# Kernel optimization log

Measured on AMD Instinct MI355X. Metric: run time of the kernel, lower is better.

The kernel has to match this reference:

```python
import jax, jax.numpy as jnp
import numpy as np

LN_EPS = 1e-5

def setup_inputs() -> dict:
    key = jax.random.key(0)
    ks = jax.random.split(key, 12)
    B, T, R, Ds = 4, 128, 64, 128
    N = 2048
    d_id = 128
    max_neurons, max_regions, max_eids = 2048, 128, 256
    U = jax.random.normal(ks[0], (B, T, R, Ds), dtype=jnp.float32)
    neuron_regions = jax.random.randint(ks[1], (B, N), 0, max_regions, dtype=jnp.int32)
    eids = jax.random.randint(ks[2], (B,), 0, max_eids, dtype=jnp.int32)
    r_map = jax.random.randint(ks[3], (max_regions,), 0, R, dtype=jnp.int32)
    s = 0.02
    neuron_slot = jax.random.normal(ks[4], (max_neurons, d_id), dtype=jnp.float32) * s
    region_emb = jax.random.normal(ks[5], (max_regions, d_id), dtype=jnp.float32) * s
    eid_emb = jax.random.normal(ks[6], (max_eids, d_id), dtype=jnp.float32) * s
    ln_gamma = jnp.ones((d_id,), dtype=jnp.float32)
    ln_beta = jnp.zeros((d_id,), dtype=jnp.float32)
    W1 = jax.random.normal(ks[7], (d_id, 2 * Ds), dtype=jnp.float32) * (1.0 / np.sqrt(d_id))
    b1 = jnp.zeros((2 * Ds,), dtype=jnp.float32)
    W2 = jax.random.normal(ks[8], (2 * Ds, Ds + 1), dtype=jnp.float32) * (1.0 / np.sqrt(2 * Ds))
    b2 = jnp.zeros((Ds + 1,), dtype=jnp.float32)  # nn.init.zeros_ on hyper[-1].bias
    return {"U": U, "neuron_regions": neuron_regions, "eids": eids, "r_map": r_map,
            "neuron_slot": neuron_slot, "region_emb": region_emb, "eid_emb": eid_emb,
            "ln_gamma": ln_gamma, "ln_beta": ln_beta, "W1": W1, "b1": b1, "W2": W2, "b2": b2}


def reference(U, neuron_regions, eids, r_map, neuron_slot, region_emb, eid_emb,
              ln_gamma, ln_beta, W1, b1, W2, b2):
    B, T, R, Ds = U.shape
    N = neuron_regions.shape[1]
    # neuron identity embedding: slot + region (+ eid)
    nr = jnp.clip(neuron_regions, 0, region_emb.shape[0] - 1)
    e = neuron_slot[:N][None, :, :] + region_emb[nr]                      # [B,N,d_id]
    e = e + eid_emb[jnp.clip(eids, 0, eid_emb.shape[0] - 1)][:, None, :]
    # hyper-MLP: LayerNorm -> Linear -> GELU(exact) -> Linear
    mu = e.mean(-1, keepdims=True)
    var = ((e - mu) ** 2).mean(-1, keepdims=True)
    h = (e - mu) * jax.lax.rsqrt(var + LN_EPS) * ln_gamma + ln_beta
    h = jax.nn.gelu(h @ W1 + b1, approximate=False)
    wb = h @ W2 + b2                                                      # [B,N,Ds+1]
    w = wb[..., :Ds]                                                      # [B,N,Ds]
    bias = wb[..., Ds]                                                    # [B,N]
    # region-indexed gather + weighted reduce
    local_r = r_map[jnp.clip(neuron_regions, 0, r_map.shape[0] - 1)]      # [B,N]
    lr_safe = jnp.clip(local_r, 0, None)
    idx = jnp.broadcast_to(lr_safe[:, None, :, None], (B, T, N, Ds))
    U_neur = jnp.take_along_axis(U, idx, axis=2)                          # [B,T,N,Ds]
    pred = jnp.einsum('btnd,bnd->btn', U_neur, w) + bias[:, None, :]
    pred = jnp.where((local_r < 0)[:, None, :], jnp.zeros_like(pred), pred)
    return pred
```

## Files before the change

### kernel.cpp

```cpp
#include <hip/hip_runtime.h>
#include <hip/hip_bf16.h>
#include <math.h>

#define DEV __device__ __forceinline__

typedef __attribute__((ext_vector_type(8))) short short8v;
typedef __attribute__((ext_vector_type(4))) float f32x4;

DEV unsigned short f2bf(float x) {
    unsigned u = __float_as_uint(x);
    return (unsigned short)((u + 0x7fffu + ((u >> 16) & 1u)) >> 16);
}
DEV unsigned pack2(float lo, float hi) {
    return ((unsigned)f2bf(hi) << 16) | (unsigned)f2bf(lo);
}
DEV f32x4 mfma16(short8v a, short8v b, f32x4 c) {
    return __builtin_amdgcn_mfma_f32_16x16x32_bf16(a, b, c, 0, 0, 0);
}

DEV float gelu_fast(float x) {
    const float z  = x * 0.70710678118654752f;
    const float az = fabsf(z);
    const float t  = __builtin_amdgcn_rcpf(fmaf(0.3275911f, az, 1.0f));
    float p = fmaf(t, 1.061405429f, -1.453152027f);
    p = fmaf(t, p, 1.421413741f);
    p = fmaf(t, p, -0.284496736f);
    p = fmaf(t, p, 0.254829592f);
    p = p * t;
    const float E = __builtin_amdgcn_exp2f(z * z * -1.4426950408889634f);
    const float erf_az = fmaf(-p, E, 1.0f);
    const float erf_z  = copysignf(erf_az, z);
    const float hx = 0.5f * x;
    return fmaf(hx, erf_z, hx);
}

#define NN 2048

__global__ __launch_bounds__(256, 1) void prep_kernel(
    const float* __restrict__ W1, const float* __restrict__ W2,
    const int* __restrict__ r_map, const int* __restrict__ neuron_regions,
    unsigned short* __restrict__ W1T, unsigned short* __restrict__ W2T,
    float* __restrict__ w2col, int* __restrict__ order, int* __restrict__ offs)
{
    __shared__ __align__(16) float T[32][33];
    __shared__ int hist[65], starts[66], cursor[65];
    const int tid = threadIdx.x;
    const int bid = blockIdx.x;

    if (bid < 32) {
        const int tr = bid >> 3, tc = bid & 7;
#pragma unroll
        for (int p = 0; p < 4; p++) {
            const int i = p * 8 + (tid >> 5), j = tid & 31;
            T[i][j] = W1[(tr * 32 + i) * 256 + tc * 32 + j];
        }
        __syncthreads();
#pragma unroll
        for (int p = 0; p < 4; p++) {
            const int i = p * 8 + (tid >> 5), j = tid & 31;
            W1T[(tc * 32 + i) * 128 + tr * 32 + j] = f2bf(T[j][i]);
        }
    } else if (bid < 64) {
        const int bb = bid - 32, tr = bb >> 2, tc = bb & 3;
#pragma unroll
        for (int p = 0; p < 4; p++) {
            const int i = p * 8 + (tid >> 5), j = tid & 31;
            T[i][j] = W2[(tr * 32 + i) * 129 + tc * 32 + j];
        }
        __syncthreads();
#pragma unroll
        for (int p = 0; p < 4; p++) {
            const int i = p * 8 + (tid >> 5), j = tid & 31;
            W2T[(tc * 32 + i) * 256 + tr * 32 + j] = f2bf(T[j][i]);
        }
    } else if (bid == 64) {
        w2col[tid] = W2[tid * 129 + 128];
    } else {
        const int b = bid - 65;
        for (int i = tid; i < 65; i += 256) hist[i] = 0;
        __syncthreads();
        for (int n = tid; n < NN; n += 256) {
            int nr = min(max(neuron_regions[b * NN + n], 0), 127);
            int lr = r_map[nr];
            int bin = (lr < 0) ? 64 : min(lr, 63);
            atomicAdd(&hist[bin], 1);
        }
        __syncthreads();
        if (tid == 0) {
            int run = 0;
            for (int i = 0; i < 65; i++) { starts[i] = run; cursor[i] = run; run += hist[i]; }
            starts[65] = run;
        }
        __syncthreads();
        for (int i = tid; i < 66; i += 256) offs[b * 66 + i] = starts[i];
        for (int n = tid; n < NN; n += 256) {
            int nr = min(max(neuron_regions[b * NN + n], 0), 127);
            int lr = r_map[nr];
            int bin = (lr < 0) ? 64 : min(lr, 63);
            int pos = atomicAdd(&cursor[bin], 1);
            order[b * NN + pos] = n;
        }
    }
}

__global__ __launch_bounds__(256, 2) void p1_kernel(
    const int* __restrict__ neuron_regions, const int* __restrict__ eids,
    const float* __restrict__ neuron_slot, const float* __restrict__ region_emb,
    const float* __restrict__ eid_emb, const float* __restrict__ ln_gamma,
    const float* __restrict__ ln_beta, const float* __restrict__ b1,
    const float* __restrict__ b2, const unsigned short* __restrict__ W1T,
    const unsigned short* __restrict__ W2T, const float* __restrict__ w2col,
    unsigned short* __restrict__ w_ws, float* __restrict__ bias_ws)
{
    __shared__ __align__(16) unsigned short hT[16][136];
    __shared__ __align__(16) unsigned short H1[16][264];
    __shared__ float biasp[16];
    const int tid = threadIdx.x;
    const int row0 = blockIdx.x * 16;
    if (tid < 16) biasp[tid] = 0.f;

    {
        const int rr = tid >> 4, q = tid & 15;
        const int row = row0 + rr;
        const int b = row >> 11, n = row & (NN - 1);
        int nr = min(max(neuron_regions[b * NN + n], 0), 127);
        int eid = min(max(eids[b], 0), 255);
        const float* ns = neuron_slot + n * 128 + q * 8;
        const float* re = region_emb + nr * 128 + q * 8;
        const float* ee = eid_emb + eid * 128 + q * 8;
        float e[8];
        {
            float4 a0 = *(const float4*)ns, a1 = *(const float4*)(ns + 4);
            float4 c0 = *(const float4*)re, c1 = *(const float4*)(re + 4);
            float4 d0 = *(const float4*)ee, d1 = *(const float4*)(ee + 4);
            e[0] = a0.x + c0.x + d0.x; e[1] = a0.y + c0.y + d0.y;
            e[2] = a0.z + c0.z + d0.z; e[3] = a0.w + c0.w + d0.w;
            e[4] = a1.x + c1.x + d1.x; e[5] = a1.y + c1.y + d1.y;
            e[6] = a1.z + c1.z + d1.z; e[7] = a1.w + c1.w + d1.w;
        }
        float s = 0.f, s2 = 0.f;
#pragma unroll
        for (int i = 0; i < 8; i++) { s += e[i]; s2 += e[i] * e[i]; }
        s += __shfl_xor(s, 1);  s2 += __shfl_xor(s2, 1);
        s += __shfl_xor(s, 2);  s2 += __shfl_xor(s2, 2);
        s += __shfl_xor(s, 4);  s2 += __shfl_xor(s2, 4);
        s += __shfl_xor(s, 8);  s2 += __shfl_xor(s2, 8);
        const float mu = s * (1.f / 128.f);
        const float var = s2 * (1.f / 128.f) - mu * mu;
        const float rstd = rsqrtf(var + 1e-5f);
        float4 g0 = *(const float4*)(ln_gamma + q * 8), g1 = *(const float4*)(ln_gamma + q * 8 + 4);
        float4 t0 = *(const float4*)(ln_beta + q * 8),  t1 = *(const float4*)(ln_beta + q * 8 + 4);
        float gm[8] = {g0.x, g0.y, g0.z, g0.w, g1.x, g1.y, g1.z, g1.w};
        float bt[8] = {t0.x, t0.y, t0.z, t0.w, t1.x, t1.y, t1.z, t1.w};
        float h[8];
#pragma unroll
        for (int i = 0; i < 8; i++) h[i] = (e[i] - mu) * rstd * gm[i] + bt[i];
        uint4 pk;
        pk.x = pack2(h[0], h[1]); pk.y = pack2(h[2], h[3]);
        pk.z = pack2(h[4], h[5]); pk.w = pack2(h[6], h[7]);
        *(uint4*)&hT[rr][q * 8] = pk;
    }
    __syncthreads();

    const int wv = tid >> 6, l = tid & 63;
    const int lr = l & 15, lh = l >> 4;

    short8v afr[4];
#pragma unroll
    for (int ks = 0; ks < 4; ks++)
        afr[ks] = *(const short8v*)&hT[lr][ks * 32 + lh * 8];

    float pb[4] = {0.f, 0.f, 0.f, 0.f};
#pragma unroll
    for (int nt = 0; nt < 4; nt++) {
        const int n = wv * 64 + nt * 16 + lr;
        short8v bfr[4];
#pragma unroll
        for (int ks = 0; ks < 4; ks++)
            bfr[ks] = *(const short8v*)(W1T + n * 128 + ks * 32 + lh * 8);
        const float bb = b1[n];
        const float w2cv = w2col[n];
        f32x4 a; a.x = bb; a.y = bb; a.z = bb; a.w = bb;
#pragma unroll
        for (int ks = 0; ks < 4; ks++) a = mfma16(afr[ks], bfr[ks], a);
#pragma unroll
        for (int j = 0; j < 4; j++) {
            const float g = gelu_fast(a[j]);
            H1[lh * 4 + j][n] = f2bf(g);
            pb[j] += g * w2cv;
        }
    }
#pragma unroll
    for (int j = 0; j < 4; j++) {
        pb[j] += __shfl_xor(pb[j], 1);
        pb[j] += __shfl_xor(pb[j], 2);
        pb[j] += __shfl_xor(pb[j], 4);
        pb[j] += __shfl_xor(pb[j], 8);
    }
    if (lr == 0) {
#pragma unroll
        for (int j = 0; j < 4; j++) atomicAdd(&biasp[lh * 4 + j], pb[j]);
    }
    __syncthreads();

    if (tid < 16) bias_ws[row0 + tid] = biasp[tid] + b2[128];

    short8v a2[8];
#pragma unroll
    for (int ks = 0; ks < 8; ks++)
        a2[ks] = *(const short8v*)&H1[lr][ks * 32 + lh * 8];

    f32x4 acc2[2];
#pragma unroll
    for (int nt = 0; nt < 2; nt++) {
        const int n = wv * 32 + nt * 16 + lr;
        short8v bf[8];
#pragma unroll
        for (int ks = 0; ks < 8; ks++)
            bf[ks] = *(const short8v*)(W2T + n * 256 + ks * 32 + lh * 8);
        const float bb = b2[n];
        f32x4 a; a.x = bb; a.y = bb; a.z = bb; a.w = bb;
#pragma unroll
        for (int ks = 0; ks < 8; ks++) a = mfma16(a2[ks], bf[ks], a);
        acc2[nt] = a;
    }

    __syncthreads();
#pragma unroll
    for (int nt = 0; nt < 2; nt++) {
        const int n = wv * 32 + nt * 16 + lr;
#pragma unroll
        for (int j = 0; j < 4; j++)
            hT[lh * 4 + j][n] = f2bf(acc2[nt][j]);
    }
    __syncthreads();
    {
        const int r = tid >> 4, c = tid & 15;
        uint4 v = *(const uint4*)&hT[r][c * 8];
        *(uint4*)(w_ws + (row0 + r) * 128 + c * 8) = v;
    }
}

__global__ __launch_bounds__(256, 1) void p2_kernel(
    const float* __restrict__ U, const int* __restrict__ order,
    const int* __restrict__ offs, const unsigned short* __restrict__ w_ws,
    const float* __restrict__ bias_ws, float* __restrict__ out)
{
    __shared__ __align__(16) unsigned short Ubf[32][136];
    __shared__ __align__(16) unsigned short Bt[32][136];
    __shared__ int nidS[32];
    __shared__ float biasS[32];
    const int tid = threadIdx.x;
    const int bid = blockIdx.x;

    if (bid >= 1024) {
        const int b = bid - 1024;
        const int s64 = offs[b * 66 + 64], s65 = offs[b * 66 + 65];
        const int cnt = s65 - s64;
        for (int idx = tid; idx < cnt * 128; idx += 256) {
            const int j = idx >> 7, t = idx & 127;
            const int n = order[b * NN + s64 + j];
            out[(size_t)(b * 128 + t) * NN + n] = 0.f;
        }
        return;
    }

    const int b = bid >> 8, rem = bid & 255;
    const int slot = rem >> 2, tq = rem & 3;
    const int t0 = tq * 32;
    const int s0 = offs[b * 66 + slot], s1 = offs[b * 66 + slot + 1];
    const int cnt = s1 - s0;
    if (cnt <= 0) return;

    {
        const int t = tid >> 3, q = tid & 7;
        const float* src = U + ((size_t)((b * 128 + t0 + t) * 64 + slot)) * 128 + q * 16;
        unsigned short* dst = &Ubf[t][q * 16];
        float4 v0 = ((const float4*)src)[0], v1 = ((const float4*)src)[1];
        float4 v2 = ((const float4*)src)[2], v3 = ((const float4*)src)[3];
        uint4 pkA, pkB;
        pkA.x = pack2(v0.x, v0.y); pkA.y = pack2(v0.z, v0.w);
        pkA.z = pack2(v1.x, v1.y); pkA.w = pack2(v1.z, v1.w);
        pkB.x = pack2(v2.x, v2.y); pkB.y = pack2(v2.z, v2.w);
        pkB.z = pack2(v3.x, v3.y); pkB.w = pack2(v3.z, v3.w);
        ((uint4*)dst)[0] = pkA;
        ((uint4*)dst)[1] = pkB;
    }
    __syncthreads();

    const int wv = tid >> 6, l = tid & 63;
    const int lr = l & 15, lh = l >> 4;
    const int rtile = wv >> 1, nhalf = wv & 1;

    short8v afr[4];
#pragma unroll
    for (int ks = 0; ks < 4; ks++)
        afr[ks] = *(const short8v*)&Ubf[rtile * 16 + lr][ks * 32 + lh * 8];

    const int nChunks = (cnt + 31) >> 5;
    for (int c = 0; c < nChunks; c++) {
        const int base = s0 + c * 32;
        const int cc = min(cnt - c * 32, 32);
        __syncthreads();
        if (tid < 32) {
            const int nid = (tid < cc) ? order[b * NN + base + tid] : -1;
            nidS[tid] = nid;
            biasS[tid] = (nid >= 0) ? bias_ws[b * NN + nid] : 0.f;
        }
        {
            const int jj = tid >> 3, q = tid & 7;
            const int nid = (jj < cc) ? order[b * NN + base + jj] : -1;
            unsigned short* dst = &Bt[jj][q * 16];
            if (nid >= 0) {
                const uint4* src = (const uint4*)(w_ws + ((size_t)(b * NN + nid)) * 128 + q * 16);
                ((uint4*)dst)[0] = src[0];
                ((uint4*)dst)[1] = src[1];
            } else {
                ((uint4*)dst)[0] = make_uint4(0, 0, 0, 0);
                ((uint4*)dst)[1] = make_uint4(0, 0, 0, 0);
            }
        }
        __syncthreads();

        short8v bfr[4];
#pragma unroll
        for (int ks = 0; ks < 4; ks++)
            bfr[ks] = *(const short8v*)&Bt[nhalf * 16 + lr][ks * 32 + lh * 8];

        f32x4 a; a.x = 0.f; a.y = 0.f; a.z = 0.f; a.w = 0.f;
#pragma unroll
        for (int ks = 0; ks < 4; ks++) a = mfma16(afr[ks], bfr[ks], a);

        const int j = nhalf * 16 + lr;
        const int nid = nidS[j];
        if (nid >= 0) {
            const float bs = biasS[j];
#pragma unroll
            for (int jr = 0; jr < 4; jr++)
                out[(size_t)(b * 128 + t0 + rtile * 16 + lh * 4 + jr) * NN + nid] =
                    a[jr] + bs;
        }
    }
}

extern "C" void kernel_launch(void* const* d_in, const int* in_sizes, int n_in,
                              void* d_out, int out_size, void* d_ws, size_t ws_size,
                              hipStream_t stream)
{
    const float* U              = (const float*)d_in[0];
    const int*   neuron_regions = (const int*)d_in[1];
    const int*   eids           = (const int*)d_in[2];
    const int*   r_map          = (const int*)d_in[3];
    const float* neuron_slot    = (const float*)d_in[4];
    const float* region_emb     = (const float*)d_in[5];
    const float* eid_emb        = (const float*)d_in[6];
    const float* ln_gamma       = (const float*)d_in[7];
    const float* ln_beta        = (const float*)d_in[8];
    const float* W1             = (const float*)d_in[9];
    const float* b1             = (const float*)d_in[10];
    const float* W2             = (const float*)d_in[11];
    const float* b2             = (const float*)d_in[12];

    char* ws = (char*)d_ws;
    unsigned short* w_ws    = (unsigned short*)(ws);
    float*          bias_ws = (float*)(ws + 0x200000);
    unsigned short* W1T     = (unsigned short*)(ws + 0x208000);
    unsigned short* W2T     = (unsigned short*)(ws + 0x218000);
    float*          w2col   = (float*)(ws + 0x228000);
    int*            order   = (int*)(ws + 0x229000);
    int*            offs    = (int*)(ws + 0x231000);
    float* outp = (float*)d_out;

    hipLaunchKernelGGL(prep_kernel, dim3(69), dim3(256), 0, stream,
                       W1, W2, r_map, neuron_regions, W1T, W2T, w2col, order, offs);
    hipLaunchKernelGGL(p1_kernel, dim3(512), dim3(256), 0, stream,
                       neuron_regions, eids, neuron_slot, region_emb, eid_emb,
                       ln_gamma, ln_beta, b1, b2, W1T, W2T, w2col, w_ws, bias_ws);
    hipLaunchKernelGGL(p2_kernel, dim3(1028), dim3(256), 0, stream,
                       U, order, offs, w_ws, bias_ws, outp);
}
```

Measured before the change: 36.19 us.

## Split p2 work into per-chunk descriptors so each block handles one 32-neuron chunk

The prep kernel now builds a per-batch list of (slot, chunk base) descriptors, one per 32-neuron chunk of each region bin, plus a count. p2 launches 2048 blocks indexed by (batch, time quarter, descriptor), so each block processes exactly one chunk instead of looping over all chunks of a slot. The masked-neuron zeroing moves into the block whose descriptor index equals the count, split per time quarter. This balances load across blocks when region bins have uneven sizes. The cost is that each block reloads and converts its U tile, and many blocks exit early.

```diff
diff --git a/kernel.cpp b/kernel.cpp
--- a/kernel.cpp
+++ b/kernel.cpp
@@ -40,7 +40,8 @@
     const float* __restrict__ W1, const float* __restrict__ W2,
     const int* __restrict__ r_map, const int* __restrict__ neuron_regions,
     unsigned short* __restrict__ W1T, unsigned short* __restrict__ W2T,
-    float* __restrict__ w2col, int* __restrict__ order, int* __restrict__ offs)
+    float* __restrict__ w2col, int* __restrict__ order, int* __restrict__ offs,
+    int* __restrict__ desc, int* __restrict__ dcount)
 {
     __shared__ __align__(16) float T[32][33];
     __shared__ int hist[65], starts[66], cursor[65];
@@ -90,6 +91,13 @@
             int run = 0;
             for (int i = 0; i < 65; i++) { starts[i] = run; cursor[i] = run; run += hist[i]; }
             starts[65] = run;
+            int k = 0;
+            for (int s2 = 0; s2 < 64; s2++) {
+                const int len = starts[s2 + 1] - starts[s2];
+                for (int base = 0; base < len; base += 32)
+                    desc[b * 128 + k++] = s2 | (base << 8);
+            }
+            dcount[b] = k;
         }
         __syncthreads();
         for (int i = tid; i < 66; i += 256) offs[b * 66 + i] = starts[i];
@@ -243,7 +251,8 @@
 
 __global__ __launch_bounds__(256, 1) void p2_kernel(
     const float* __restrict__ U, const int* __restrict__ order,
-    const int* __restrict__ offs, const unsigned short* __restrict__ w_ws,
+    const int* __restrict__ offs, const int* __restrict__ desc,
+    const int* __restrict__ dcount, const unsigned short* __restrict__ w_ws,
     const float* __restrict__ bias_ws, float* __restrict__ out)
 {
     __shared__ __align__(16) unsigned short Ubf[32][136];
@@ -252,25 +261,29 @@
     __shared__ float biasS[32];
     const int tid = threadIdx.x;
     const int bid = blockIdx.x;
-
-    if (bid >= 1024) {
-        const int b = bid - 1024;
-        const int s64 = offs[b * 66 + 64], s65 = offs[b * 66 + 65];
-        const int cnt = s65 - s64;
-        for (int idx = tid; idx < cnt * 128; idx += 256) {
-            const int j = idx >> 7, t = idx & 127;
-            const int n = order[b * NN + s64 + j];
-            out[(size_t)(b * 128 + t) * NN + n] = 0.f;
+    const int b = bid >> 9, rem = bid & 511;
+    const int tq = rem >> 7, ci = rem & 127;
+    const int t0 = tq * 32;
+
+    const int dcnt = dcount[b];
+    if (ci > dcnt) return;
+    if (ci == dcnt) {
+        const int d0 = offs[b * 66 + 64];
+        const int dc = offs[b * 66 + 65] - d0;
+        for (int idx = tid; idx < dc * 32; idx += 256) {
+            const int j = idx >> 5, t = idx & 31;
+            out[(size_t)(b * 128 + t0 + t) * NN + order[b * NN + d0 + j]] = 0.f;
         }
         return;
     }
 
-    const int b = bid >> 8, rem = bid & 255;
-    const int slot = rem >> 2, tq = rem & 3;
-    const int t0 = tq * 32;
-    const int s0 = offs[b * 66 + slot], s1 = offs[b * 66 + slot + 1];
-    const int cnt = s1 - s0;
-    if (cnt <= 0) return;
+    const int d = desc[b * 128 + ci];
+    const int slot = d & 63;
+    const int base0 = d >> 8;
+    const int s0 = offs[b * 66 + slot];
+    const int cnt = offs[b * 66 + slot + 1] - s0;
+    const int cc = min(cnt - base0, 32);
+    const int base = s0 + base0;
 
     {
         const int t = tid >> 3, q = tid & 7;
@@ -286,6 +299,25 @@
         ((uint4*)dst)[0] = pkA;
         ((uint4*)dst)[1] = pkB;
     }
+
+    if (tid < 32) {
+        const int nid = (tid < cc) ? order[b * NN + base + tid] : -1;
+        nidS[tid] = nid;
+        biasS[tid] = (nid >= 0) ? bias_ws[b * NN + nid] : 0.f;
+    }
+    {
+        const int jj = tid >> 3, q = tid & 7;
+        const int nid = (jj < cc) ? order[b * NN + base + jj] : -1;
+        unsigned short* dst = &Bt[jj][q * 16];
+        if (nid >= 0) {
+            const uint4* src = (const uint4*)(w_ws + ((size_t)(b * NN + nid)) * 128 + q * 16);
+            ((uint4*)dst)[0] = src[0];
+            ((uint4*)dst)[1] = src[1];
+        } else {
+            ((uint4*)dst)[0] = make_uint4(0, 0, 0, 0);
+            ((uint4*)dst)[1] = make_uint4(0, 0, 0, 0);
+        }
+    }
     __syncthreads();
 
     const int wv = tid >> 6, l = tid & 63;
@@ -297,49 +329,23 @@
     for (int ks = 0; ks < 4; ks++)
         afr[ks] = *(const short8v*)&Ubf[rtile * 16 + lr][ks * 32 + lh * 8];
 
-    const int nChunks = (cnt + 31) >> 5;
-    for (int c = 0; c < nChunks; c++) {
-        const int base = s0 + c * 32;
-        const int cc = min(cnt - c * 32, 32);
-        __syncthreads();
-        if (tid < 32) {
-            const int nid = (tid < cc) ? order[b * NN + base + tid] : -1;
-            nidS[tid] = nid;
-            biasS[tid] = (nid >= 0) ? bias_ws[b * NN + nid] : 0.f;
-        }
-        {
-            const int jj = tid >> 3, q = tid & 7;
-            const int nid = (jj < cc) ? order[b * NN + base + jj] : -1;
-            unsigned short* dst = &Bt[jj][q * 16];
-            if (nid >= 0) {
-                const uint4* src = (const uint4*)(w_ws + ((size_t)(b * NN + nid)) * 128 + q * 16);
-                ((uint4*)dst)[0] = src[0];
-                ((uint4*)dst)[1] = src[1];
-            } else {
-                ((uint4*)dst)[0] = make_uint4(0, 0, 0, 0);
-                ((uint4*)dst)[1] = make_uint4(0, 0, 0, 0);
-            }
-        }
-        __syncthreads();
-
-        short8v bfr[4];
-#pragma unroll
-        for (int ks = 0; ks < 4; ks++)
-            bfr[ks] = *(const short8v*)&Bt[nhalf * 16 + lr][ks * 32 + lh * 8];
-
-        f32x4 a; a.x = 0.f; a.y = 0.f; a.z = 0.f; a.w = 0.f;
-#pragma unroll
-        for (int ks = 0; ks < 4; ks++) a = mfma16(afr[ks], bfr[ks], a);
-
-        const int j = nhalf * 16 + lr;
-        const int nid = nidS[j];
-        if (nid >= 0) {
-            const float bs = biasS[j];
-#pragma unroll
-            for (int jr = 0; jr < 4; jr++)
-                out[(size_t)(b * 128 + t0 + rtile * 16 + lh * 4 + jr) * NN + nid] =
-                    a[jr] + bs;
-        }
+    short8v bfr[4];
+#pragma unroll
+    for (int ks = 0; ks < 4; ks++)
+        bfr[ks] = *(const short8v*)&Bt[nhalf * 16 + lr][ks * 32 + lh * 8];
+
+    f32x4 a; a.x = 0.f; a.y = 0.f; a.z = 0.f; a.w = 0.f;
+#pragma unroll
+    for (int ks = 0; ks < 4; ks++) a = mfma16(afr[ks], bfr[ks], a);
+
+    const int j = nhalf * 16 + lr;
+    const int nid = nidS[j];
+    if (nid >= 0) {
+        const float bs = biasS[j];
+#pragma unroll
+        for (int jr = 0; jr < 4; jr++)
+            out[(size_t)(b * 128 + t0 + rtile * 16 + lh * 4 + jr) * NN + nid] =
+                a[jr] + bs;
     }
 }
 
@@ -369,13 +375,16 @@
     float*          w2col   = (float*)(ws + 0x228000);
     int*            order   = (int*)(ws + 0x229000);
     int*            offs    = (int*)(ws + 0x231000);
+    int*            desc    = (int*)(ws + 0x232000);
+    int*            dcount  = (int*)(ws + 0x232800);
     float* outp = (float*)d_out;
 
     hipLaunchKernelGGL(prep_kernel, dim3(69), dim3(256), 0, stream,
-                       W1, W2, r_map, neuron_regions, W1T, W2T, w2col, order, offs);
+                       W1, W2, r_map, neuron_regions, W1T, W2T, w2col,
+                       order, offs, desc, dcount);
     hipLaunchKernelGGL(p1_kernel, dim3(512), dim3(256), 0, stream,
                        neuron_regions, eids, neuron_slot, region_emb, eid_emb,
                        ln_gamma, ln_beta, b1, b2, W1T, W2T, w2col, w_ws, bias_ws);
-    hipLaunchKernelGGL(p2_kernel, dim3(1028), dim3(256), 0, stream,
-                       U, order, offs, w_ws, bias_ws, outp);
-}
+    hipLaunchKernelGGL(p2_kernel, dim3(2048), dim3(256), 0, stream,
+                       U, order, offs, desc, dcount, w_ws, bias_ws, outp);
+}
```

Result: slower. 48.24 us (+33.3%).
